# Kernel optimization log

Measured on AMD Instinct MI355X. Metric: run time of the kernel, lower is better.

## Reference

```python
import jax, jax.numpy as jnp
import numpy as np
from jax import lax

EPS_COS = 1e-8  # torch F.cosine_similarity eps
EPS_GN = 1e-5   # torch GroupNorm eps


def setup_inputs() -> dict:
    key = jax.random.key(0)
    k1, k2, k3 = jax.random.split(key, 3)
    b, f, h, w = 4, 64, 64, 64
    fdm = jax.random.uniform(k1, (b, 1, 2 * h, 2 * w), dtype=jnp.float32)
    x = jax.random.normal(k2, (b, f, h, w), dtype=jnp.float32)
    W_fuse = jax.random.normal(k3, (f, 2 * f, 3, 3), dtype=jnp.float32) * 0.05
    b_fuse = jnp.zeros((f,), jnp.float32)
    gamma = jnp.ones((f,), jnp.float32)
    beta = jnp.zeros((f,), jnp.float32)
    return {"fdm": fdm, "x": x, "W_fuse": W_fuse, "b_fuse": b_fuse,
            "gamma": gamma, "beta": beta}


def reference(fdm, x, W_fuse, b_fuse, gamma, beta):
    b, f, h, w = x.shape
    # adaptive_max_pool2d(fdm, (h, w)): input spatial is exact multiple -> plain max pool
    kh, kw = fdm.shape[2] // h, fdm.shape[3] // w
    fdm_p = lax.reduce_window(fdm, -jnp.inf, lax.max,
                              (1, 1, kh, kw), (1, 1, kh, kw), 'VALID')  # [b,1,h,w]
    # per-sample threshold: min(0.5, max(fdm)/3)
    maxv = jnp.max(fdm_p, axis=(1, 2, 3))                 # [b]
    thre = jnp.minimum(0.5, maxv / 3.0)                   # [b]
    mask = fdm_p.reshape(b, h * w) >= thre[:, None]       # [b, HW] selected pixels

    # cosine similarity between selected feature vectors and all positions.
    # Original masked-selects N rows then computes N x HW sims and max-reduces over N;
    # we compute the full HW x HW sim and mask unselected rows to -inf (same max).
    xf = x.reshape(b, f, h * w).transpose(0, 2, 1)        # [b, HW, f]
    norm = jnp.sqrt(jnp.sum(xf * xf, axis=-1, keepdims=True))
    xn = xf / jnp.maximum(norm, EPS_COS)
    sim = jnp.einsum('bpf,bqf->bpq', xn, xn)              # [b, HW(sel), HW(all)]
    sim = jnp.where(mask[:, :, None], sim, -jnp.inf)
    sm = (jnp.max(sim, axis=1) / 2.0 + 0.5).reshape(b, 1, h, w)

    # fuse: Conv2d(2f -> f, k3, pad1) + GroupNorm(1, f) + ReLU
    cat = jnp.concatenate([sm * x, x], axis=1)            # [b, 2f, h, w]
    y = lax.conv_general_dilated(cat, W_fuse, (1, 1), 'SAME',
                                 dimension_numbers=('NCHW', 'OIHW', 'NCHW'))
    y = y + b_fuse[None, :, None, None]
    mu = jnp.mean(y, axis=(1, 2, 3), keepdims=True)
    var = jnp.mean((y - mu) ** 2, axis=(1, 2, 3), keepdims=True)
    y = (y - mu) / jnp.sqrt(var + EPS_GN)
    y = y * gamma[None, :, None, None] + beta[None, :, None, None]
    x0 = jax.nn.relu(y)
    return x0, sm
```

## Files before the change

kernel.cpp:

```cpp
#include <hip/hip_runtime.h>
#include <math.h>


#define HW 4096
#define NCH 64

typedef __attribute__((ext_vector_type(8))) short short8;
typedef __attribute__((ext_vector_type(4))) float f32x4;

static __device__ __forceinline__ ushort f2bf(float f) {
    unsigned u = __float_as_uint(f);
    unsigned r = (u + 0x7fffu + ((u >> 16) & 1u)) >> 16;
    return (ushort)r;
}
static __device__ __forceinline__ float bf2f(ushort h) {
    return __uint_as_float(((unsigned)h) << 16);
}
static __device__ __forceinline__ unsigned mapf(float f) {
    unsigned u = __float_as_uint(f);
    return u ^ ((unsigned)((int)u >> 31) | 0x80000000u);
}
static __device__ __forceinline__ float unmapf(unsigned u) {
    unsigned b = (u & 0x80000000u) ? (u ^ 0x80000000u) : ~u;
    return __uint_as_float(b);
}

__global__ __launch_bounds__(256) void k_pnp(
    const float* __restrict__ fdm, const float* __restrict__ x,
    float* __restrict__ pooledOut, float* __restrict__ threOut,
    int* __restrict__ unsel, int* __restrict__ unselN,
    float* __restrict__ gnS1, float* __restrict__ gnS2,
    float* __restrict__ rn, float* __restrict__ smOut, ushort* __restrict__ inb) {
    const int t = threadIdx.x;
    if (blockIdx.x < 4) {
        const int b = blockIdx.x;
        __shared__ float pooled[4096];
        __shared__ float red[256];
        __shared__ int cnt;
        const float* fb = fdm + b * 16384;
        float lmax = -1.0f;
#pragma unroll
        for (int it = 0; it < 8; ++it) {
            int id2 = it * 256 + t;
            int i = id2 >> 5;
            int j2 = id2 & 31;
            const float* base = fb + i * 256 + j2 * 4;
            float4 a = *(const float4*)base;
            float4 c = *(const float4*)(base + 128);
            float p0 = fmaxf(fmaxf(a.x, a.y), fmaxf(c.x, c.y));
            float p1 = fmaxf(fmaxf(a.z, a.w), fmaxf(c.z, c.w));
            pooled[i * 64 + j2 * 2]     = p0;
            pooled[i * 64 + j2 * 2 + 1] = p1;
            lmax = fmaxf(lmax, fmaxf(p0, p1));
        }
        red[t] = lmax;
        __syncthreads();
        for (int s = 128; s > 0; s >>= 1) {
            if (t < s) red[t] = fmaxf(red[t], red[t + s]);
            __syncthreads();
        }
        __shared__ float thre_s;
        if (t == 0) {
            thre_s = fminf(0.5f, red[0] / 3.0f);
            cnt = 0;
            gnS1[b] = 0.0f; gnS2[b] = 0.0f;
        }
        __syncthreads();
        const float th = thre_s;
#pragma unroll
        for (int it = 0; it < 4; ++it) {
            int idx = (it * 256 + t) * 4;
            *(float4*)(pooledOut + b * 4096 + idx) = *(const float4*)(pooled + idx);
        }
        for (int idx = t; idx < 4096; idx += 256) {
            if (!(pooled[idx] >= th)) {
                int pos = atomicAdd(&cnt, 1);
                unsel[b * 4096 + pos] = idx;
            }
        }
        __syncthreads();
        if (t == 0) { unselN[b] = cnt; threOut[b] = th; }
    } else {
        __shared__ float s_part[4][64];
        const int n = blockIdx.x - 4;
        const int b = n >> 6;
        const int pbase = (n & 63) * 64;
        const int wv = t >> 6;
        const int l = t & 63;
        const int sp = pbase + l;
        const float* xp = x + b * (NCH * HW) + sp;
        float xv[16];
        float ss = 0.f;
#pragma unroll
        for (int i = 0; i < 16; ++i) {
            float a = xp[(wv * 16 + i) * HW];
            xv[i] = a;
            ss += a * a;
        }
        s_part[wv][l] = ss;
        ushort h[16];
#pragma unroll
        for (int i = 0; i < 16; ++i) h[i] = f2bf(xv[i]);
        size_t dst1 = ((size_t)(b * 8 + wv) * 4096 + sp) * 16;
        size_t dst2 = ((size_t)(b * 8 + 4 + wv) * 4096 + sp) * 16;
        *(uint4*)(inb + dst1)     = *(const uint4*)h;
        *(uint4*)(inb + dst1 + 8) = *(const uint4*)(h + 8);
        *(uint4*)(inb + dst2)     = *(const uint4*)h;
        *(uint4*)(inb + dst2 + 8) = *(const uint4*)(h + 8);
        __syncthreads();
        if (t < 64) {
            float s = s_part[0][l] + s_part[1][l] + s_part[2][l] + s_part[3][l];
            int g = b * HW + pbase + l;
            rn[g] = 1.0f / fmaxf(sqrtf(s), 1e-8f);
            smOut[g] = 1.0f;
        }
    }
}

__global__ void k_qgw(const float* __restrict__ x, const float* __restrict__ rn,
                      const int* __restrict__ unsel, const int* __restrict__ unselN,
                      ushort* __restrict__ qmh, ushort* __restrict__ qml, unsigned* __restrict__ scores,
                      const float* __restrict__ W, ushort* __restrict__ wbh, ushort* __restrict__ wbl) {
    const int t = threadIdx.x;
    if (blockIdx.x < 4) {
        const int b = blockIdx.x;
        const int nu = unselN[b];
        for (int qi = t; qi < nu; qi += 256) scores[b * 4096 + qi] = 0u;
        for (int idx = t; idx < nu * 64; idx += 256) {
            int qi = idx >> 6;
            int c = idx & 63;
            int q = unsel[b * 4096 + qi];
            float rq = rn[b * 4096 + q];
            float v = x[b * (NCH * HW) + c * HW + q] * rq;
            ushort hb = f2bf(v);
            size_t o = ((size_t)(b * 4096) + qi) * 64 + c;
            qmh[o] = hb;
            qml[o] = f2bf(v - bf2f(hb));
        }
    } else {
        const int u = (blockIdx.x - 4) * 256 + t;
        const int tap = u >> 10;
        const int rem = u & 1023;
        const int oc = rem >> 4;
        const int g = rem & 15;
        ushort hh[8], ll[8];
#pragma unroll
        for (int j = 0; j < 8; ++j) {
            int ic = g * 8 + j;
            float v = W[(oc * 128 + ic) * 9 + tap];
            ushort hb = f2bf(v);
            hh[j] = hb;
            ll[j] = f2bf(v - bf2f(hb));
        }
        *(uint4*)(wbh + (size_t)u * 8) = *(const uint4*)hh;
        *(uint4*)(wbl + (size_t)u * 8) = *(const uint4*)ll;
    }
}

__global__ __launch_bounds__(256, 1) void k_score(
    const ushort* __restrict__ inb, const ushort* __restrict__ qmh, const ushort* __restrict__ qml,
    const float* __restrict__ rn, const float* __restrict__ pooledM, const float* __restrict__ threArr,
    const int* __restrict__ unselN, unsigned* __restrict__ scores) {
    const int b = blockIdx.y;
    const int n0 = blockIdx.x * 128;
    const int t = threadIdx.x;
    const int lane = t & 63;
    const int wave = t >> 6;
    const int li = lane & 15;
    const int quad = lane >> 4;
    const int nu = unselN[b];

    __shared__ __align__(16) ushort s_xp[128 * 72];
    __shared__ __align__(16) ushort s_qh[64 * 72];
    __shared__ __align__(16) ushort s_ql[64 * 72];
    __shared__ float s_rp[128];
    __shared__ float s_neg[128];
    __shared__ unsigned s_best[64];

    for (int idx = t; idx < 1024; idx += 256) {
        int p_l = idx >> 3;
        int g = (idx >> 1) & 3;
        int sub = idx & 1;
        uint4 v = *(const uint4*)(inb + (((size_t)(b * 8 + 4 + g) * 4096) + n0 + p_l) * 16 + sub * 8);
        *(uint4*)(s_xp + p_l * 72 + g * 16 + sub * 8) = v;
    }
    if (t < 128) {
        int p = n0 + t;
        s_rp[t] = rn[b * 4096 + p];
        s_neg[t] = (pooledM[b * 4096 + p] >= threArr[b]) ? 0.0f : -INFINITY;
    }

    for (int qs0 = 0; qs0 < nu; qs0 += 64) {
        __syncthreads();
        for (int idx = t; idx < 512; idx += 256) {
            int q_l = idx >> 3;
            int sub = idx & 7;
            int q_g = qs0 + q_l; if (q_g > 4095) q_g = 4095;
            size_t src = ((size_t)(b * 4096) + q_g) * 64 + sub * 8;
            *(uint4*)(s_qh + q_l * 72 + sub * 8) = *(const uint4*)(qmh + src);
            *(uint4*)(s_ql + q_l * 72 + sub * 8) = *(const uint4*)(qml + src);
        }
        if (t < 64) s_best[t] = 0u;
        __syncthreads();

        f32x4 acc[2][4];
#pragma unroll
        for (int nt = 0; nt < 2; ++nt)
#pragma unroll
            for (int mt = 0; mt < 4; ++mt) acc[nt][mt] = (f32x4){0.f, 0.f, 0.f, 0.f};
#pragma unroll
        for (int k0 = 0; k0 < 2; ++k0) {
            short8 b0 = *(const short8*)(s_xp + ((size_t)((2 * wave) * 16 + li)) * 72 + k0 * 32 + quad * 8);
            short8 b1 = *(const short8*)(s_xp + ((size_t)((2 * wave + 1) * 16 + li)) * 72 + k0 * 32 + quad * 8);
#pragma unroll
            for (int mt = 0; mt < 4; ++mt) {
                short8 ah = *(const short8*)(s_qh + ((size_t)(mt * 16 + li)) * 72 + k0 * 32 + quad * 8);
                short8 al = *(const short8*)(s_ql + ((size_t)(mt * 16 + li)) * 72 + k0 * 32 + quad * 8);
                acc[0][mt] = __builtin_amdgcn_mfma_f32_16x16x32_bf16(ah, b0, acc[0][mt], 0, 0, 0);
                acc[0][mt] = __builtin_amdgcn_mfma_f32_16x16x32_bf16(al, b0, acc[0][mt], 0, 0, 0);
                acc[1][mt] = __builtin_amdgcn_mfma_f32_16x16x32_bf16(ah, b1, acc[1][mt], 0, 0, 0);
                acc[1][mt] = __builtin_amdgcn_mfma_f32_16x16x32_bf16(al, b1, acc[1][mt], 0, 0, 0);
            }
        }
        const float rp0 = s_rp[(2 * wave) * 16 + li];
        const float ng0 = s_neg[(2 * wave) * 16 + li];
        const float rp1 = s_rp[(2 * wave + 1) * 16 + li];
        const float ng1 = s_neg[(2 * wave + 1) * 16 + li];
#pragma unroll
        for (int mt = 0; mt < 4; ++mt) {
#pragma unroll
            for (int r = 0; r < 4; ++r) {
                float sc = fmaxf(acc[0][mt][r] * rp0 + ng0, acc[1][mt][r] * rp1 + ng1);
                sc = fmaxf(sc, __shfl_xor(sc, 1));
                sc = fmaxf(sc, __shfl_xor(sc, 2));
                sc = fmaxf(sc, __shfl_xor(sc, 4));
                sc = fmaxf(sc, __shfl_xor(sc, 8));
                if (li == 0) atomicMax(&s_best[mt * 16 + quad * 4 + r], mapf(sc));
            }
        }
        __syncthreads();
        if (t < 64 && qs0 + t < nu) atomicMax(scores + b * 4096 + qs0 + t, s_best[t]);
    }
}

__global__ void k_fixup(const float* __restrict__ x, const int* __restrict__ unsel,
                        const int* __restrict__ unselN, const unsigned* __restrict__ scores,
                        float* __restrict__ smOut, ushort* __restrict__ inb) {
    const int b = blockIdx.x;
    const int t = threadIdx.x;
    const int nu = unselN[b];
    __shared__ float s_sm[4096];
    for (int qi = t; qi < nu; qi += 256) {
        float sm = unmapf(scores[b * 4096 + qi]) * 0.5f + 0.5f;
        s_sm[qi] = sm;
        smOut[b * 4096 + unsel[b * 4096 + qi]] = sm;
    }
    __syncthreads();
    for (int idx = t; idx < nu * 64; idx += 256) {
        int qi = idx >> 6;
        int c = idx & 63;
        int q = unsel[b * 4096 + qi];
        float v = x[b * (NCH * HW) + c * HW + q] * s_sm[qi];
        inb[(((size_t)(b * 8 + (c >> 4)) * 4096) + q) * 16 + (c & 15)] = f2bf(v);
    }
}

__global__ __launch_bounds__(256) void k_conv_mfma(
    const ushort* __restrict__ inb, const ushort* __restrict__ wbh, const ushort* __restrict__ wbl,
    const float* __restrict__ bfuse, float* __restrict__ y,
    float* __restrict__ gnS1, float* __restrict__ gnS2) {
    const int rowblk = blockIdx.x;
    const int ocblk = blockIdx.y;
    const int b = blockIdx.z;
    const int t = threadIdx.x;
    const int lane = t & 63;
    const int wave = t >> 6;
    const int li = lane & 15;
    const int quad = lane >> 4;
    const int h0 = rowblk * 4;
    const int oc0 = ocblk * 16;

    __shared__ __align__(16) ushort s_in[6 * 66 * 40];
    __shared__ __align__(16) ushort s_wh[9 * 16 * 40];
    __shared__ __align__(16) ushort s_wl[9 * 16 * 40];
    __shared__ float red1[256];
    __shared__ float red2[256];

    f32x4 acc[4];
#pragma unroll
    for (int j = 0; j < 4; ++j) acc[j] = (f32x4){0.f, 0.f, 0.f, 0.f};

    for (int chunk = 0; chunk < 4; ++chunk) {
        __syncthreads();
        for (int idx = t; idx < 1584; idx += 256) {
            int part = idx & 3;
            int cell = idx >> 2;
            int r = cell / 66;
            int c = cell - r * 66;
            int h = h0 + r - 1;
            int w = c - 1;
            uint4 v = make_uint4(0u, 0u, 0u, 0u);
            if ((unsigned)h < 64u && (unsigned)w < 64u) {
                int grp = 2 * chunk + (part >> 1);
                int sub = part & 1;
                v = *(const uint4*)(inb + (((size_t)(b * 8 + grp) * 4096 + h * 64 + w) * 16 + sub * 8));
            }
            *(uint4*)(s_in + (size_t)cell * 40 + part * 8) = v;
        }
        const int ic0 = chunk * 32;
        for (int idx = t; idx < 1152; idx += 256) {
            int part = idx & 3;
            int uu = idx >> 2;
            int hl = uu / 144;
            int rem = uu - hl * 144;
            int tap = rem >> 4;
            int o = rem & 15;
            const ushort* src = (hl ? wbl : wbh) + ((size_t)(tap * 64 + oc0 + o) * 128 + ic0 + part * 8);
            uint4 v = *(const uint4*)src;
            ushort* dst = (hl ? s_wl : s_wh) + ((size_t)(tap * 16 + o) * 40 + part * 8);
            *(uint4*)dst = v;
        }
        __syncthreads();
#pragma unroll
        for (int kh = 0; kh < 3; ++kh) {
            const int r = wave + kh;
#pragma unroll
            for (int kw = 0; kw < 3; ++kw) {
                const int tap = kh * 3 + kw;
                short8 ah = *(const short8*)(s_wh + (size_t)(tap * 16 + li) * 40 + quad * 8);
                short8 al = *(const short8*)(s_wl + (size_t)(tap * 16 + li) * 40 + quad * 8);
#pragma unroll
                for (int j = 0; j < 4; ++j) {
                    int c = j * 16 + li + kw;
                    short8 bv = *(const short8*)(s_in + ((size_t)(r * 66 + c) * 40 + quad * 8));
                    acc[j] = __builtin_amdgcn_mfma_f32_16x16x32_bf16(ah, bv, acc[j], 0, 0, 0);
                    acc[j] = __builtin_amdgcn_mfma_f32_16x16x32_bf16(al, bv, acc[j], 0, 0, 0);
                }
            }
        }
    }
    float bias[4];
#pragma unroll
    for (int reg = 0; reg < 4; ++reg) bias[reg] = bfuse[oc0 + quad * 4 + reg];
    float s1 = 0.f, s2 = 0.f;
    const int hrow = h0 + wave;
#pragma unroll
    for (int j = 0; j < 4; ++j) {
#pragma unroll
        for (int reg = 0; reg < 4; ++reg) {
            float v = acc[j][reg] + bias[reg];
            y[((size_t)(b * 64 + oc0 + quad * 4 + reg)) * HW + hrow * 64 + j * 16 + li] = v;
            s1 += v; s2 += v * v;
        }
    }
    red1[t] = s1; red2[t] = s2;
    __syncthreads();
    for (int s = 128; s > 0; s >>= 1) {
        if (t < s) { red1[t] += red1[t + s]; red2[t] += red2[t + s]; }
        __syncthreads();
    }
    if (t == 0) {
        atomicAdd(&gnS1[b], red1[0]);
        atomicAdd(&gnS2[b], red2[0]);
    }
}

__global__ void k_gn(float* __restrict__ out, const float* __restrict__ gnS1, const float* __restrict__ gnS2,
                     const float* __restrict__ gamma, const float* __restrict__ beta) {
    const int e = (blockIdx.x * 256 + threadIdx.x) * 4;
    const int b = e >> 18;
    const int c = (e >> 12) & 63;
    const float inv = 1.0f / 262144.0f;
    float mu = gnS1[b] * inv;
    float var = gnS2[b] * inv - mu * mu;
    float rs = rsqrtf(var + 1e-5f);
    float scale = rs * gamma[c];
    float shift = beta[c] - mu * scale;
    float4 v = *(const float4*)(out + e);
    float4 o;
    o.x = fmaxf(v.x * scale + shift, 0.0f);
    o.y = fmaxf(v.y * scale + shift, 0.0f);
    o.z = fmaxf(v.z * scale + shift, 0.0f);
    o.w = fmaxf(v.w * scale + shift, 0.0f);
    *(float4*)(out + e) = o;
}

extern "C" void kernel_launch(void* const* d_in, const int* in_sizes, int n_in,
                              void* d_out, int out_size, void* d_ws, size_t ws_size,
                              hipStream_t stream) {
    const float* fdm   = (const float*)d_in[0];
    const float* x     = (const float*)d_in[1];
    const float* Wf    = (const float*)d_in[2];
    const float* bfuse = (const float*)d_in[3];
    const float* gamma = (const float*)d_in[4];
    const float* beta  = (const float*)d_in[5];
    float* out = (float*)d_out;
    float* ws  = (float*)d_ws;

    float*    rn      = ws;
    float*    pooledM = rn + 16384;
    int*      unsel   = (int*)(pooledM + 16384);
    unsigned* scores  = (unsigned*)(unsel + 16384);
    float*    thre    = (float*)(scores + 16384);
    int*      unselN  = (int*)(thre + 4);
    float*    gnS1    = (float*)(unselN + 4);
    float*    gnS2    = gnS1 + 4;
    ushort*   wbh     = (ushort*)(gnS2 + 4);
    ushort*   wbl     = wbh + 73728;
    ushort*   qmh     = wbl + 73728;
    ushort*   qml     = qmh + 1048576;
    ushort*   inb     = qml + 1048576;

    float* yout  = out;
    float* smOut = out + 1048576;

    k_pnp<<<dim3(260), dim3(256), 0, stream>>>(fdm, x, pooledM, thre, unsel, unselN,
                                               gnS1, gnS2, rn, smOut, inb);
    k_qgw<<<dim3(40), dim3(256), 0, stream>>>(x, rn, unsel, unselN, qmh, qml, scores, Wf, wbh, wbl);
    k_score<<<dim3(32, 4), dim3(256), 0, stream>>>(inb, qmh, qml, rn, pooledM, thre, unselN, scores);
    k_fixup<<<dim3(4), dim3(256), 0, stream>>>(x, unsel, unselN, scores, smOut, inb);
    k_conv_mfma<<<dim3(16, 4, 4), dim3(256), 0, stream>>>(inb, wbh, wbl, bfuse, yout, gnS1, gnS2);
    k_gn<<<dim3(1024), dim3(256), 0, stream>>>(yout, gnS1, gnS2, gamma, beta);
}
```

Measured before the change: 120.8 us.

## Fuse query gather, score zeroing and sm fixup into neighbouring kernels

Drops the k_qgw and k_fixup kernels. Weight conversion and score zeroing move into k_pnp. k_score now gathers and normalises the unselected query vectors straight from x into shared memory, and reads the pixel operands directly from global memory instead of staging them. k_conv_mfma applies the similarity scaling to the haloed input tile in shared memory and writes smOut for unselected pixels. This removes two launches and the qmh/qml intermediates, at the cost of redundant gather and scale work repeated in each score and conv block.

```diff
diff --git a/kernel.cpp b/kernel.cpp
--- a/kernel.cpp
+++ b/kernel.cpp
@@ -26,11 +26,12 @@
 }
 
 __global__ __launch_bounds__(256) void k_pnp(
-    const float* __restrict__ fdm, const float* __restrict__ x,
+    const float* __restrict__ fdm, const float* __restrict__ x, const float* __restrict__ W,
     float* __restrict__ pooledOut, float* __restrict__ threOut,
-    int* __restrict__ unsel, int* __restrict__ unselN,
+    int* __restrict__ unsel, int* __restrict__ unselN, unsigned* __restrict__ scores,
     float* __restrict__ gnS1, float* __restrict__ gnS2,
-    float* __restrict__ rn, float* __restrict__ smOut, ushort* __restrict__ inb) {
+    float* __restrict__ rn, float* __restrict__ smOut, ushort* __restrict__ inb,
+    ushort* __restrict__ wbh, ushort* __restrict__ wbl) {
     const int t = threadIdx.x;
     if (blockIdx.x < 4) {
         const int b = blockIdx.x;
@@ -73,6 +74,7 @@
             *(float4*)(pooledOut + b * 4096 + idx) = *(const float4*)(pooled + idx);
         }
         for (int idx = t; idx < 4096; idx += 256) {
+            scores[b * 4096 + idx] = 0u;
             if (!(pooled[idx] >= th)) {
                 int pos = atomicAdd(&cnt, 1);
                 unsel[b * 4096 + pos] = idx;
@@ -80,7 +82,7 @@
         }
         __syncthreads();
         if (t == 0) { unselN[b] = cnt; threOut[b] = th; }
-    } else {
+    } else if (blockIdx.x < 260) {
         __shared__ float s_part[4][64];
         const int n = blockIdx.x - 4;
         const int b = n >> 6;
@@ -114,31 +116,8 @@
             rn[g] = 1.0f / fmaxf(sqrtf(s), 1e-8f);
             smOut[g] = 1.0f;
         }
-    }
-}
-
-__global__ void k_qgw(const float* __restrict__ x, const float* __restrict__ rn,
-                      const int* __restrict__ unsel, const int* __restrict__ unselN,
-                      ushort* __restrict__ qmh, ushort* __restrict__ qml, unsigned* __restrict__ scores,
-                      const float* __restrict__ W, ushort* __restrict__ wbh, ushort* __restrict__ wbl) {
-    const int t = threadIdx.x;
-    if (blockIdx.x < 4) {
-        const int b = blockIdx.x;
-        const int nu = unselN[b];
-        for (int qi = t; qi < nu; qi += 256) scores[b * 4096 + qi] = 0u;
-        for (int idx = t; idx < nu * 64; idx += 256) {
-            int qi = idx >> 6;
-            int c = idx & 63;
-            int q = unsel[b * 4096 + qi];
-            float rq = rn[b * 4096 + q];
-            float v = x[b * (NCH * HW) + c * HW + q] * rq;
-            ushort hb = f2bf(v);
-            size_t o = ((size_t)(b * 4096) + qi) * 64 + c;
-            qmh[o] = hb;
-            qml[o] = f2bf(v - bf2f(hb));
-        }
     } else {
-        const int u = (blockIdx.x - 4) * 256 + t;
+        const int u = (blockIdx.x - 260) * 256 + t;
         const int tap = u >> 10;
         const int rem = u & 1023;
         const int oc = rem >> 4;
@@ -157,10 +136,11 @@
     }
 }
 
-__global__ __launch_bounds__(256, 1) void k_score(
-    const ushort* __restrict__ inb, const ushort* __restrict__ qmh, const ushort* __restrict__ qml,
-    const float* __restrict__ rn, const float* __restrict__ pooledM, const float* __restrict__ threArr,
-    const int* __restrict__ unselN, unsigned* __restrict__ scores) {
+__global__ __launch_bounds__(256) void k_score(
+    const float* __restrict__ x, const float* __restrict__ rn,
+    const float* __restrict__ pooledM, const float* __restrict__ threArr,
+    const int* __restrict__ unsel, const int* __restrict__ unselN,
+    const ushort* __restrict__ inb, unsigned* __restrict__ scores) {
     const int b = blockIdx.y;
     const int n0 = blockIdx.x * 128;
     const int t = threadIdx.x;
@@ -169,36 +149,34 @@
     const int li = lane & 15;
     const int quad = lane >> 4;
     const int nu = unselN[b];
-
-    __shared__ __align__(16) ushort s_xp[128 * 72];
+    if (nu == 0) return;
+
     __shared__ __align__(16) ushort s_qh[64 * 72];
     __shared__ __align__(16) ushort s_ql[64 * 72];
-    __shared__ float s_rp[128];
-    __shared__ float s_neg[128];
     __shared__ unsigned s_best[64];
 
-    for (int idx = t; idx < 1024; idx += 256) {
-        int p_l = idx >> 3;
-        int g = (idx >> 1) & 3;
-        int sub = idx & 1;
-        uint4 v = *(const uint4*)(inb + (((size_t)(b * 8 + 4 + g) * 4096) + n0 + p_l) * 16 + sub * 8);
-        *(uint4*)(s_xp + p_l * 72 + g * 16 + sub * 8) = v;
-    }
-    if (t < 128) {
-        int p = n0 + t;
-        s_rp[t] = rn[b * 4096 + p];
-        s_neg[t] = (pooledM[b * 4096 + p] >= threArr[b]) ? 0.0f : -INFINITY;
-    }
+    const float th = threArr[b];
+    const int p0 = n0 + (2 * wave) * 16 + li;
+    const int p1 = n0 + (2 * wave + 1) * 16 + li;
+    const float rp0 = rn[b * 4096 + p0];
+    const float rp1 = rn[b * 4096 + p1];
+    const float ng0 = (pooledM[b * 4096 + p0] >= th) ? 0.0f : -INFINITY;
+    const float ng1 = (pooledM[b * 4096 + p1] >= th) ? 0.0f : -INFINITY;
 
     for (int qs0 = 0; qs0 < nu; qs0 += 64) {
         __syncthreads();
-        for (int idx = t; idx < 512; idx += 256) {
-            int q_l = idx >> 3;
-            int sub = idx & 7;
-            int q_g = qs0 + q_l; if (q_g > 4095) q_g = 4095;
-            size_t src = ((size_t)(b * 4096) + q_g) * 64 + sub * 8;
-            *(uint4*)(s_qh + q_l * 72 + sub * 8) = *(const uint4*)(qmh + src);
-            *(uint4*)(s_ql + q_l * 72 + sub * 8) = *(const uint4*)(qml + src);
+        for (int idx = t; idx < 4096; idx += 256) {
+            int q_l = idx >> 6;
+            int c = idx & 63;
+            int qg = qs0 + q_l;
+            float v = 0.0f;
+            if (qg < nu) {
+                int q = unsel[b * 4096 + qg];
+                v = x[b * (NCH * HW) + c * HW + q] * rn[b * 4096 + q];
+            }
+            ushort hb = f2bf(v);
+            s_qh[q_l * 72 + c] = hb;
+            s_ql[q_l * 72 + c] = f2bf(v - bf2f(hb));
         }
         if (t < 64) s_best[t] = 0u;
         __syncthreads();
@@ -210,22 +188,21 @@
             for (int mt = 0; mt < 4; ++mt) acc[nt][mt] = (f32x4){0.f, 0.f, 0.f, 0.f};
 #pragma unroll
         for (int k0 = 0; k0 < 2; ++k0) {
-            short8 b0 = *(const short8*)(s_xp + ((size_t)((2 * wave) * 16 + li)) * 72 + k0 * 32 + quad * 8);
-            short8 b1 = *(const short8*)(s_xp + ((size_t)((2 * wave + 1) * 16 + li)) * 72 + k0 * 32 + quad * 8);
+            const int cb = k0 * 32 + quad * 8;
+            const int grp = 4 + (cb >> 4);
+            const int sub = cb & 15;
+            short8 b0 = *(const short8*)(inb + (((size_t)(b * 8 + grp) * 4096) + p0) * 16 + sub);
+            short8 b1 = *(const short8*)(inb + (((size_t)(b * 8 + grp) * 4096) + p1) * 16 + sub);
 #pragma unroll
             for (int mt = 0; mt < 4; ++mt) {
-                short8 ah = *(const short8*)(s_qh + ((size_t)(mt * 16 + li)) * 72 + k0 * 32 + quad * 8);
-                short8 al = *(const short8*)(s_ql + ((size_t)(mt * 16 + li)) * 72 + k0 * 32 + quad * 8);
+                short8 ah = *(const short8*)(s_qh + (size_t)(mt * 16 + li) * 72 + cb);
+                short8 al = *(const short8*)(s_ql + (size_t)(mt * 16 + li) * 72 + cb);
                 acc[0][mt] = __builtin_amdgcn_mfma_f32_16x16x32_bf16(ah, b0, acc[0][mt], 0, 0, 0);
                 acc[0][mt] = __builtin_amdgcn_mfma_f32_16x16x32_bf16(al, b0, acc[0][mt], 0, 0, 0);
                 acc[1][mt] = __builtin_amdgcn_mfma_f32_16x16x32_bf16(ah, b1, acc[1][mt], 0, 0, 0);
                 acc[1][mt] = __builtin_amdgcn_mfma_f32_16x16x32_bf16(al, b1, acc[1][mt], 0, 0, 0);
             }
         }
-        const float rp0 = s_rp[(2 * wave) * 16 + li];
-        const float ng0 = s_neg[(2 * wave) * 16 + li];
-        const float rp1 = s_rp[(2 * wave + 1) * 16 + li];
-        const float ng1 = s_neg[(2 * wave + 1) * 16 + li];
 #pragma unroll
         for (int mt = 0; mt < 4; ++mt) {
 #pragma unroll
@@ -243,32 +220,11 @@
     }
 }
 
-__global__ void k_fixup(const float* __restrict__ x, const int* __restrict__ unsel,
-                        const int* __restrict__ unselN, const unsigned* __restrict__ scores,
-                        float* __restrict__ smOut, ushort* __restrict__ inb) {
-    const int b = blockIdx.x;
-    const int t = threadIdx.x;
-    const int nu = unselN[b];
-    __shared__ float s_sm[4096];
-    for (int qi = t; qi < nu; qi += 256) {
-        float sm = unmapf(scores[b * 4096 + qi]) * 0.5f + 0.5f;
-        s_sm[qi] = sm;
-        smOut[b * 4096 + unsel[b * 4096 + qi]] = sm;
-    }
-    __syncthreads();
-    for (int idx = t; idx < nu * 64; idx += 256) {
-        int qi = idx >> 6;
-        int c = idx & 63;
-        int q = unsel[b * 4096 + qi];
-        float v = x[b * (NCH * HW) + c * HW + q] * s_sm[qi];
-        inb[(((size_t)(b * 8 + (c >> 4)) * 4096) + q) * 16 + (c & 15)] = f2bf(v);
-    }
-}
-
 __global__ __launch_bounds__(256) void k_conv_mfma(
     const ushort* __restrict__ inb, const ushort* __restrict__ wbh, const ushort* __restrict__ wbl,
-    const float* __restrict__ bfuse, float* __restrict__ y,
-    float* __restrict__ gnS1, float* __restrict__ gnS2) {
+    const float* __restrict__ bfuse, const int* __restrict__ unsel, const int* __restrict__ unselN,
+    const unsigned* __restrict__ scores, float* __restrict__ smOut,
+    float* __restrict__ y, float* __restrict__ gnS1, float* __restrict__ gnS2) {
     const int rowblk = blockIdx.x;
     const int ocblk = blockIdx.y;
     const int b = blockIdx.z;
@@ -279,12 +235,20 @@
     const int quad = lane >> 4;
     const int h0 = rowblk * 4;
     const int oc0 = ocblk * 16;
+    const int nu = unselN[b];
 
     __shared__ __align__(16) ushort s_in[6 * 66 * 40];
     __shared__ __align__(16) ushort s_wh[9 * 16 * 40];
     __shared__ __align__(16) ushort s_wl[9 * 16 * 40];
     __shared__ float red1[256];
     __shared__ float red2[256];
+
+    if (rowblk == 0 && ocblk == 0) {
+        for (int qi = t; qi < nu; qi += 256) {
+            float sm = unmapf(scores[b * 4096 + qi]) * 0.5f + 0.5f;
+            smOut[b * 4096 + unsel[b * 4096 + qi]] = sm;
+        }
+    }
 
     f32x4 acc[4];
 #pragma unroll
@@ -319,6 +283,25 @@
             uint4 v = *(const uint4*)src;
             ushort* dst = (hl ? s_wl : s_wh) + ((size_t)(tap * 16 + o) * 40 + part * 8);
             *(uint4*)dst = v;
+        }
+        if (chunk < 2) {
+            __syncthreads();
+            for (int idx = t; idx < nu * 4; idx += 256) {
+                int qi = idx >> 2;
+                int part = idx & 3;
+                int q = unsel[b * 4096 + qi];
+                int hq = q >> 6, wq = q & 63;
+                int r = hq - h0 + 1;
+                if ((unsigned)r < 6u) {
+                    float sm = unmapf(scores[b * 4096 + qi]) * 0.5f + 0.5f;
+                    ushort* ptr = s_in + (size_t)(r * 66 + wq + 1) * 40 + part * 8;
+                    ushort hv[8];
+                    *(uint4*)hv = *(const uint4*)ptr;
+#pragma unroll
+                    for (int j = 0; j < 8; ++j) hv[j] = f2bf(bf2f(hv[j]) * sm);
+                    *(uint4*)ptr = *(const uint4*)hv;
+                }
+            }
         }
         __syncthreads();
 #pragma unroll
@@ -407,18 +390,15 @@
     float*    gnS2    = gnS1 + 4;
     ushort*   wbh     = (ushort*)(gnS2 + 4);
     ushort*   wbl     = wbh + 73728;
-    ushort*   qmh     = wbl + 73728;
-    ushort*   qml     = qmh + 1048576;
-    ushort*   inb     = qml + 1048576;
+    ushort*   inb     = wbl + 73728;
 
     float* yout  = out;
     float* smOut = out + 1048576;
 
-    k_pnp<<<dim3(260), dim3(256), 0, stream>>>(fdm, x, pooledM, thre, unsel, unselN,
-                                               gnS1, gnS2, rn, smOut, inb);
-    k_qgw<<<dim3(40), dim3(256), 0, stream>>>(x, rn, unsel, unselN, qmh, qml, scores, Wf, wbh, wbl);
-    k_score<<<dim3(32, 4), dim3(256), 0, stream>>>(inb, qmh, qml, rn, pooledM, thre, unselN, scores);
-    k_fixup<<<dim3(4), dim3(256), 0, stream>>>(x, unsel, unselN, scores, smOut, inb);
-    k_conv_mfma<<<dim3(16, 4, 4), dim3(256), 0, stream>>>(inb, wbh, wbl, bfuse, yout, gnS1, gnS2);
+    k_pnp<<<dim3(296), dim3(256), 0, stream>>>(fdm, x, Wf, pooledM, thre, unsel, unselN,
+                                               scores, gnS1, gnS2, rn, smOut, inb, wbh, wbl);
+    k_score<<<dim3(32, 4), dim3(256), 0, stream>>>(x, rn, pooledM, thre, unsel, unselN, inb, scores);
+    k_conv_mfma<<<dim3(16, 4, 4), dim3(256), 0, stream>>>(inb, wbh, wbl, bfuse, unsel, unselN,
+                                                          scores, smOut, yout, gnS1, gnS2);
     k_gn<<<dim3(1024), dim3(256), 0, stream>>>(yout, gnS1, gnS2, gamma, beta);
 }
```

Measured after the change: 114.4 us. 1.06x faster.
